# Kernel optimization log

Measured on AMD Instinct MI355X. Metric: run time of the kernel, lower is better.

The kernel has to match this reference:

```python
import jax, jax.numpy as jnp
import numpy as np

B, L, D = 16, 8192, 256

def setup_inputs() -> dict:
    key = jax.random.key(0)
    inputs = jax.random.normal(key, (B, L, D), dtype=jnp.float32)
    return {"inputs": inputs}

def reference(inputs) -> jnp.ndarray:
    # position weights: softmax over L of per-token L2 norms
    norms = jnp.linalg.norm(inputs, axis=2)            # [B, L]
    w = jax.nn.softmax(norms, axis=1)                  # [B, L]
    # weighted sum of outer products == X^T diag(w) X, fused as one einsum
    out = jnp.einsum('bl,bld,ble->bde', w, inputs, inputs)  # [B, D, D]
    return out
```

## Files before the change

### kernel.cpp

```cpp
#include <hip/hip_runtime.h>
#include <hip/hip_bf16.h>

#define NB 16
#define NL 8192
#define ND 256

#define KSPLIT 32
#define BK 64
#define KSTRIDE 72

#define WS_G_OFF 131328

typedef __bf16 bf16_t;
typedef __attribute__((ext_vector_type(8))) __bf16 bf16x8;
typedef __attribute__((ext_vector_type(4))) float floatx4;

__global__ __launch_bounds__(256, 4) void k_gemm(const float* __restrict__ x,
                                                 float* __restrict__ ws,
                                                 float* __restrict__ gram) {
    const int ks = blockIdx.x;
    const int tp = blockIdx.y;
    const int b  = blockIdx.z;
    const int t = threadIdx.x;
    const int wave = t >> 6, lane = t & 63;

    const int acolb = (tp == 2) ? 128 : 0;
    const int bcolb = (tp == 0) ? 0 : 128;

    __shared__ bf16_t lds[256 * KSTRIDE];

    const float* xb = x + (size_t)b * NL * ND;
    const int l0 = ks * (NL / KSPLIT);

    floatx4 acc[2][8];
    #pragma unroll
    for (int rt = 0; rt < 2; ++rt)
        #pragma unroll
        for (int ct = 0; ct < 8; ++ct)
            #pragma unroll
            for (int r = 0; r < 4; ++r) acc[rt][ct][r] = 0.f;

    float e_acc = 0.f;

    for (int kk = 0; kk < NL / KSPLIT; kk += BK) {
        __syncthreads();
        #pragma unroll
        for (int i = 0; i < 2; ++i) {
            const int u  = t + i * 256;
            const int cg = u & 63;
            const int kg = u >> 6;
            const int lrow = l0 + kk + kg * 8;
            const float* gp = xb + (size_t)lrow * ND + cg * 4;
            bf16x8 p[4];
            #pragma unroll
            for (int h = 0; h < 2; ++h) {
                float4 v[4]; float ss[4];
                #pragma unroll
                for (int j = 0; j < 4; ++j) {
                    v[j] = *(const float4*)(gp + (size_t)(h * 4 + j) * ND);
                    ss[j] = v[j].x * v[j].x + v[j].y * v[j].y
                          + v[j].z * v[j].z + v[j].w * v[j].w;
                }
                #pragma unroll
                for (int off = 32; off; off >>= 1) {
                    #pragma unroll
                    for (int j = 0; j < 4; ++j) ss[j] += __shfl_xor(ss[j], off, 64);
                }
                #pragma unroll
                for (int j = 0; j < 4; ++j) {
                    const float s = __expf(0.5f * sqrtf(ss[j]));
                    e_acc += s * s;
                    const float* vf = (const float*)&v[j];
                    #pragma unroll
                    for (int c = 0; c < 4; ++c)
                        p[c][h * 4 + j] = (bf16_t)(vf[c] * s);
                }
            }
            #pragma unroll
            for (int c = 0; c < 4; ++c)
                *(bf16x8*)(lds + (4 * cg + c) * KSTRIDE + kg * 8) = p[c];
        }
        __syncthreads();
        #pragma unroll
        for (int k2 = 0; k2 < 2; ++k2) {
            const int koff = k2 * 32 + (lane >> 4) * 8;
            bf16x8 af[2], bfr[8];
            #pragma unroll
            for (int rt = 0; rt < 2; ++rt) {
                const int col = acolb + (wave * 2 + rt) * 16 + (lane & 15);
                af[rt] = *(const bf16x8*)(lds + col * KSTRIDE + koff);
            }
            #pragma unroll
            for (int ct = 0; ct < 8; ++ct) {
                const int col = bcolb + ct * 16 + (lane & 15);
                bfr[ct] = *(const bf16x8*)(lds + col * KSTRIDE + koff);
            }
            #pragma unroll
            for (int rt = 0; rt < 2; ++rt)
                #pragma unroll
                for (int ct = 0; ct < 8; ++ct)
                    acc[rt][ct] = __builtin_amdgcn_mfma_f32_16x16x32_bf16(
                        af[rt], bfr[ct], acc[rt][ct], 0, 0, 0);
        }
    }

    if (tp == 0) {
        __shared__ float red[4];
        if (lane == 0) red[wave] = e_acc;
        __syncthreads();
        if (t == 0) atomicAdd(&ws[b * 16], red[0] + red[1] + red[2] + red[3]);
    }

    float* wq = gram + (size_t)((ks * 3 + tp) * 16 + b) * 16384;
    #pragma unroll
    for (int rt = 0; rt < 2; ++rt) {
        const int d0 = (wave * 2 + rt) * 16 + (lane >> 4) * 4;
        #pragma unroll
        for (int ct = 0; ct < 8; ++ct) {
            const int e = ct * 16 + (lane & 15);
            #pragma unroll
            for (int reg = 0; reg < 4; ++reg)
                wq[(size_t)(d0 + reg) * 128 + e] = acc[rt][ct][reg];
        }
    }
}

__global__ __launch_bounds__(256) void k_reduce(const float* __restrict__ gram,
                                                const float* __restrict__ ws,
                                                float* __restrict__ out) {
    const int gid = blockIdx.x * 256 + threadIdx.x;
    const int idx = gid & 16383;
    const int q   = gid >> 14;
    const int tp  = q / 16;
    const int b   = q % 16;
    const float rz = 1.0f / ws[b * 16];
    float sum = 0.f;
    #pragma unroll
    for (int ks = 0; ks < KSPLIT; ++ks)
        sum += gram[(size_t)((ks * 3 + tp) * 16 + b) * 16384 + idx];
    sum *= rz;
    const int d = idx >> 7, e = idx & 127;
    float* ob = out + (size_t)b * ND * ND;
    if (tp == 0) {
        ob[(size_t)d * ND + e] = sum;
    } else if (tp == 2) {
        ob[(size_t)(128 + d) * ND + 128 + e] = sum;
    } else {
        ob[(size_t)d * ND + 128 + e] = sum;
        ob[(size_t)(128 + e) * ND + d] = sum;
    }
}

extern "C" void kernel_launch(void* const* d_in, const int* in_sizes, int n_in,
                              void* d_out, int out_size, void* d_ws, size_t ws_size,
                              hipStream_t stream) {
    const float* x = (const float*)d_in[0];
    float* out = (float*)d_out;
    float* ws = (float*)d_ws;
    float* gram = ws + WS_G_OFF;

    hipMemsetAsync(d_ws, 0, 1024, stream);
    k_gemm<<<dim3(KSPLIT, 3, NB), 256, 0, stream>>>(x, ws, gram);
    k_reduce<<<dim3(3 * NB * 16384 / 256), 256, 0, stream>>>(gram, ws, out);
}
```

Before: 253.5 us.

## Compute symmetric Gram with circulant tile mapping, single pass over X per block

Each block now covers the whole 256x256 Gram for one L-chunk with 8 waves. Each wave owns a row tile and computes 9 or 8 circulant-offset 16x16 tiles, so only the upper triangle (136 tiles) is computed. Before, three blocks per chunk each re-read X and recomputed the norms. The LDS uses an XOR swizzle instead of padding, the next tile's global loads are prefetched into registers during the MFMA phase, and KSPLIT is halved. The reduce kernel maps the circulant tile slots back to the output and mirrors them. The cost is more registers per thread (512 threads, 2 blocks per CU) and a smaller grid of 256 blocks.

```diff
diff --git a/kernel.cpp b/kernel.cpp
--- a/kernel.cpp
+++ b/kernel.cpp
@@ -4,124 +4,132 @@
 #define NB 16
 #define NL 8192
 #define ND 256
+#define KSPLIT 16
+#define CHUNK (NL / KSPLIT)
+#define BK 64
 
-#define KSPLIT 32
-#define BK 64
-#define KSTRIDE 72
-
-#define WS_G_OFF 131328
+#define WS_G_OFF 256
 
 typedef __bf16 bf16_t;
 typedef __attribute__((ext_vector_type(8))) __bf16 bf16x8;
 typedef __attribute__((ext_vector_type(4))) float floatx4;
 
-__global__ __launch_bounds__(256, 4) void k_gemm(const float* __restrict__ x,
+__device__ __forceinline__ int fsw(int col) {
+    return ((col >> 2) & 7) ^ ((col & 3) << 1);
+}
+
+__global__ __launch_bounds__(512, 2) void k_gemm(const float* __restrict__ x,
                                                  float* __restrict__ ws,
                                                  float* __restrict__ gram) {
-    const int ks = blockIdx.x;
-    const int tp = blockIdx.y;
-    const int b  = blockIdx.z;
+    const int ks = blockIdx.x, b = blockIdx.y;
     const int t = threadIdx.x;
-    const int wave = t >> 6, lane = t & 63;
+    const int lane = t & 63;
+    const int w = __builtin_amdgcn_readfirstlane(t >> 6);
+    const int quad = lane >> 4, m = lane & 15;
 
-    const int acolb = (tp == 2) ? 128 : 0;
-    const int bcolb = (tp == 0) ? 0 : 128;
-
-    __shared__ bf16_t lds[256 * KSTRIDE];
+    __shared__ bf16_t lds[256 * 64];
 
     const float* xb = x + (size_t)b * NL * ND;
-    const int l0 = ks * (NL / KSPLIT);
+    const int l0 = ks * CHUNK;
 
-    floatx4 acc[2][8];
+    floatx4 accA[9], accB[8];
     #pragma unroll
-    for (int rt = 0; rt < 2; ++rt)
+    for (int j = 0; j < 9; ++j)
         #pragma unroll
-        for (int ct = 0; ct < 8; ++ct)
-            #pragma unroll
-            for (int r = 0; r < 4; ++r) acc[rt][ct][r] = 0.f;
+        for (int r = 0; r < 4; ++r) accA[j][r] = 0.f;
+    #pragma unroll
+    for (int j = 0; j < 8; ++j)
+        #pragma unroll
+        for (int r = 0; r < 4; ++r) accB[j][r] = 0.f;
 
     float e_acc = 0.f;
+    float4 xv[8];
 
-    for (int kk = 0; kk < NL / KSPLIT; kk += BK) {
-        __syncthreads();
+    {
+        const float* gp = xb + (size_t)(l0 + w * 8) * ND + lane * 4;
         #pragma unroll
-        for (int i = 0; i < 2; ++i) {
-            const int u  = t + i * 256;
-            const int cg = u & 63;
-            const int kg = u >> 6;
-            const int lrow = l0 + kk + kg * 8;
-            const float* gp = xb + (size_t)lrow * ND + cg * 4;
+        for (int j = 0; j < 8; ++j) xv[j] = *(const float4*)(gp + (size_t)j * ND);
+    }
+
+    for (int kk = 0; kk < CHUNK; kk += BK) {
+        if (kk) __syncthreads();
+        {
+            float ss[8];
+            #pragma unroll
+            for (int j = 0; j < 8; ++j)
+                ss[j] = xv[j].x * xv[j].x + xv[j].y * xv[j].y
+                      + xv[j].z * xv[j].z + xv[j].w * xv[j].w;
+            #pragma unroll
+            for (int off = 32; off; off >>= 1) {
+                #pragma unroll
+                for (int j = 0; j < 8; ++j) ss[j] += __shfl_xor(ss[j], off, 64);
+            }
+            float s[8];
+            #pragma unroll
+            for (int j = 0; j < 8; ++j) {
+                s[j] = __expf(0.5f * sqrtf(ss[j]));
+                e_acc += s[j] * s[j];
+            }
             bf16x8 p[4];
             #pragma unroll
-            for (int h = 0; h < 2; ++h) {
-                float4 v[4]; float ss[4];
+            for (int j = 0; j < 8; ++j) {
+                const float* vf = (const float*)&xv[j];
                 #pragma unroll
-                for (int j = 0; j < 4; ++j) {
-                    v[j] = *(const float4*)(gp + (size_t)(h * 4 + j) * ND);
-                    ss[j] = v[j].x * v[j].x + v[j].y * v[j].y
-                          + v[j].z * v[j].z + v[j].w * v[j].w;
-                }
-                #pragma unroll
-                for (int off = 32; off; off >>= 1) {
-                    #pragma unroll
-                    for (int j = 0; j < 4; ++j) ss[j] += __shfl_xor(ss[j], off, 64);
-                }
-                #pragma unroll
-                for (int j = 0; j < 4; ++j) {
-                    const float s = __expf(0.5f * sqrtf(ss[j]));
-                    e_acc += s * s;
-                    const float* vf = (const float*)&v[j];
-                    #pragma unroll
-                    for (int c = 0; c < 4; ++c)
-                        p[c][h * 4 + j] = (bf16_t)(vf[c] * s);
-                }
+                for (int c = 0; c < 4; ++c) p[c][j] = (bf16_t)(vf[c] * s[j]);
             }
             #pragma unroll
-            for (int c = 0; c < 4; ++c)
-                *(bf16x8*)(lds + (4 * cg + c) * KSTRIDE + kg * 8) = p[c];
+            for (int c = 0; c < 4; ++c) {
+                const int col = 4 * lane + c;
+                const int chunk = w ^ fsw(col);
+                *(bf16x8*)(&lds[col * 64 + chunk * 8]) = p[c];
+            }
         }
         __syncthreads();
+        if (kk + BK < CHUNK) {
+            const float* gp = xb + (size_t)(l0 + kk + BK + w * 8) * ND + lane * 4;
+            #pragma unroll
+            for (int j = 0; j < 8; ++j) xv[j] = *(const float4*)(gp + (size_t)j * ND);
+        }
         #pragma unroll
         for (int k2 = 0; k2 < 2; ++k2) {
-            const int koff = k2 * 32 + (lane >> 4) * 8;
-            bf16x8 af[2], bfr[8];
+            const int kcq = k2 * 4 + quad;
+            bf16x8 fB[16];
             #pragma unroll
-            for (int rt = 0; rt < 2; ++rt) {
-                const int col = acolb + (wave * 2 + rt) * 16 + (lane & 15);
-                af[rt] = *(const bf16x8*)(lds + col * KSTRIDE + koff);
+            for (int j = 0; j < 16; ++j) {
+                const int col = (((w + j) & 15) << 4) + m;
+                fB[j] = *(const bf16x8*)(&lds[(col << 6) + ((kcq ^ fsw(col)) << 3)]);
             }
             #pragma unroll
-            for (int ct = 0; ct < 8; ++ct) {
-                const int col = bcolb + ct * 16 + (lane & 15);
-                bfr[ct] = *(const bf16x8*)(lds + col * KSTRIDE + koff);
-            }
+            for (int j = 0; j < 9; ++j)
+                accA[j] = __builtin_amdgcn_mfma_f32_16x16x32_bf16(fB[0], fB[j], accA[j], 0, 0, 0);
             #pragma unroll
-            for (int rt = 0; rt < 2; ++rt)
-                #pragma unroll
-                for (int ct = 0; ct < 8; ++ct)
-                    acc[rt][ct] = __builtin_amdgcn_mfma_f32_16x16x32_bf16(
-                        af[rt], bfr[ct], acc[rt][ct], 0, 0, 0);
+            for (int j = 0; j < 8; ++j)
+                accB[j] = __builtin_amdgcn_mfma_f32_16x16x32_bf16(fB[8], fB[8 + j], accB[j], 0, 0, 0);
         }
     }
 
-    if (tp == 0) {
-        __shared__ float red[4];
-        if (lane == 0) red[wave] = e_acc;
-        __syncthreads();
-        if (t == 0) atomicAdd(&ws[b * 16], red[0] + red[1] + red[2] + red[3]);
+    __shared__ float red[8];
+    if (lane == 0) red[w] = e_acc;
+    __syncthreads();
+    if (t == 0) {
+        float z = 0.f;
+        #pragma unroll
+        for (int i = 0; i < 8; ++i) z += red[i];
+        atomicAdd(&ws[b * 16], z);
     }
 
-    float* wq = gram + (size_t)((ks * 3 + tp) * 16 + b) * 16384;
+    float* gb = gram + (size_t)(ks * NB + b) * 144 * 256;
     #pragma unroll
-    for (int rt = 0; rt < 2; ++rt) {
-        const int d0 = (wave * 2 + rt) * 16 + (lane >> 4) * 4;
+    for (int j = 0; j < 9; ++j) {
+        float* tb = gb + (w * 9 + j) * 256 + quad * 64 + m;
         #pragma unroll
-        for (int ct = 0; ct < 8; ++ct) {
-            const int e = ct * 16 + (lane & 15);
-            #pragma unroll
-            for (int reg = 0; reg < 4; ++reg)
-                wq[(size_t)(d0 + reg) * 128 + e] = acc[rt][ct][reg];
-        }
+        for (int reg = 0; reg < 4; ++reg) tb[reg * 16] = accA[j][reg];
+    }
+    #pragma unroll
+    for (int j = 0; j < 8; ++j) {
+        float* tb = gb + ((w + 8) * 9 + j) * 256 + quad * 64 + m;
+        #pragma unroll
+        for (int reg = 0; reg < 4; ++reg) tb[reg * 16] = accB[j][reg];
     }
 }
 
@@ -129,26 +137,24 @@
                                                 const float* __restrict__ ws,
                                                 float* __restrict__ out) {
     const int gid = blockIdx.x * 256 + threadIdx.x;
-    const int idx = gid & 16383;
-    const int q   = gid >> 14;
-    const int tp  = q / 16;
-    const int b   = q % 16;
-    const float rz = 1.0f / ws[b * 16];
+    const int elem = gid & 255;
+    const int rem  = gid >> 8;
+    const int slot = rem % 144;
+    const int b    = rem / 144;
+    const int rt = slot / 9;
+    const int j  = slot - rt * 9;
+    if (rt >= 8 && j == 8) return;
+    const int ct = (rt + j) & 15;
     float sum = 0.f;
     #pragma unroll
     for (int ks = 0; ks < KSPLIT; ++ks)
-        sum += gram[(size_t)((ks * 3 + tp) * 16 + b) * 16384 + idx];
-    sum *= rz;
-    const int d = idx >> 7, e = idx & 127;
+        sum += gram[((size_t)(ks * NB + b) * 144 + slot) * 256 + elem];
+    sum *= 1.0f / ws[b * 16];
+    const int er = elem >> 4, ec = elem & 15;
+    const int d = rt * 16 + er, e = ct * 16 + ec;
     float* ob = out + (size_t)b * ND * ND;
-    if (tp == 0) {
-        ob[(size_t)d * ND + e] = sum;
-    } else if (tp == 2) {
-        ob[(size_t)(128 + d) * ND + 128 + e] = sum;
-    } else {
-        ob[(size_t)d * ND + 128 + e] = sum;
-        ob[(size_t)(128 + e) * ND + d] = sum;
-    }
+    ob[(size_t)d * ND + e] = sum;
+    if (j) ob[(size_t)e * ND + d] = sum;
 }
 
 extern "C" void kernel_launch(void* const* d_in, const int* in_sizes, int n_in,
@@ -160,6 +166,6 @@
     float* gram = ws + WS_G_OFF;
 
     hipMemsetAsync(d_ws, 0, 1024, stream);
-    k_gemm<<<dim3(KSPLIT, 3, NB), 256, 0, stream>>>(x, ws, gram);
-    k_reduce<<<dim3(3 * NB * 16384 / 256), 256, 0, stream>>>(gram, ws, out);
+    k_gemm<<<dim3(KSPLIT, NB), 512, 0, stream>>>(x, ws, gram);
+    k_reduce<<<dim3(NB * 144 * 256 / 256), 256, 0, stream>>>(gram, ws, out);
 }
```

Measured after the change: 207.7 us. 1.22x faster.
